# Kernel tuning notes

Hardware: AMD Instinct MI355X
Metric: run time of the kernel (lower is better)

## Reference

```python
import math
import jax, jax.numpy as jnp
import numpy as np
from jax import lax

CELL_SIZE = 8
N_BINS = 9
SIGNED = False


def _conv3x3(x, k):
    # x: [N,1,H,W], k: [1,1,3,3]; padding=1 (SAME), stride 1
    return lax.conv_general_dilated(
        x, k, window_strides=(1, 1), padding=[(1, 1), (1, 1)],
        dimension_numbers=("NCHW", "OIHW", "NCHW"))


def setup_inputs() -> dict:
    key = jax.random.key(0)
    x = jax.random.uniform(key, (64, 1, 512, 512), dtype=jnp.float32)
    sobel_x = jnp.array([[-1., 0., 1.], [-2., 0., 2.], [-1., 0., 1.]],
                        dtype=jnp.float32).reshape(1, 1, 3, 3)
    sobel_y = jnp.array([[-1., -2., -1.], [0., 0., 0.], [1., 2., 1.]],
                        dtype=jnp.float32).reshape(1, 1, 3, 3)
    return {"x": x, "sobel_x": sobel_x, "sobel_y": sobel_y}


def reference(x, sobel_x, sobel_y):
    n, _, H, W = x.shape
    angle_range = 2 * math.pi if SIGNED else math.pi

    gx = _conv3x3(x, sobel_x)  # [N,1,H,W]
    gy = _conv3x3(x, sobel_y)
    mag = jnp.sqrt(gx * gx + gy * gy)          # [N,1,H,W]
    ang = jnp.arctan2(gx, gy)                  # note: atan2(gx, gy) as in source
    ang = ang + math.pi if SIGNED else jnp.abs(ang)
    bins = jnp.floor(ang / angle_range * (N_BINS - 1)).astype(jnp.int32)  # [N,1,H,W]

    # scatter_(dim=1): one-hot write of magnitudes into bin channel
    onehot = jax.nn.one_hot(bins[:, 0], N_BINS, axis=1, dtype=mag.dtype)  # [N,nb,H,W]
    out = onehot * mag                                                     # [N,nb,H,W]

    # AvgPool2d(cell,stride=cell) * cell**2 == sum over each cell
    cs = CELL_SIZE
    hog = out.reshape(n, N_BINS, H // cs, cs, W // cs, cs).sum(axis=(3, 5))
    return hog.reshape(-1)
```

## Files before the change

### kernel.cpp

```cpp
#include <hip/hip_runtime.h>
#include <math.h>

#define IMG_H 512
#define IMG_W 512
#define NB 9

__global__ __launch_bounds__(256, 4) void hog_kernel(const float* __restrict__ x,
                                                     float* __restrict__ out) {
#pragma clang fp contract(off)
    const int tid  = threadIdx.x;
    const int w    = tid >> 6;
    const int lane = tid & 63;
    const int cl   = lane & 15;
    const int qid  = lane >> 4;
    const int sr   = qid >> 1;
    const int sc   = qid & 1;

    const int cx = (w << 4) | cl;
    const int cy = blockIdx.x;
    const int n  = blockIdx.y;

    const float* img = x + (size_t)n * (IMG_H * IMG_W);
    const int x0 = (cx << 3) + (sc << 2);
    const int y0 = (cy << 3) + (sr << 2);

    float r[6][6];
#pragma unroll
    for (int i = 0; i < 6; ++i) {
        const int y = y0 - 1 + i;
        if (y < 0 || y >= IMG_H) {
#pragma unroll
            for (int j = 0; j < 6; ++j) r[i][j] = 0.0f;
        } else {
            const float* row = img + (size_t)y * IMG_W;
            const float4 p = *(const float4*)(row + x0);
            r[i][1] = p.x; r[i][2] = p.y; r[i][3] = p.z; r[i][4] = p.w;
            r[i][0] = (x0 == 0)           ? 0.0f : row[x0 - 1];
            r[i][5] = (x0 + 4 >= IMG_W)   ? 0.0f : row[x0 + 4];
        }
    }

    float accA[4], accB[4], acc8;
#pragma unroll
    for (int k = 0; k < 4; ++k) { accA[k] = 0.0f; accB[k] = 0.0f; }
    acc8 = 0.0f;

    const float PI_F = 3.14159274101257324f;
    const float T1F  = 0.41421356237309503f;
    const float T3F  = 2.41421356237309503f;
    const float KPI  = 2.54647909f;
    const float EPS  = 5e-5f;

#pragma unroll
    for (int ry = 0; ry < 4; ++ry) {
#pragma unroll
        for (int j = 0; j < 4; ++j) {
            const float A0 = r[ry][j],     A1 = r[ry][j + 1], A2 = r[ry][j + 2];
            const float B0 = r[ry + 1][j],                    B2 = r[ry + 1][j + 2];
            const float C0 = r[ry + 2][j], C1 = r[ry + 2][j + 1], C2 = r[ry + 2][j + 2];

            const float gx = ((-A0 + (A2 - 2.0f * B0)) + (2.0f * B2 - C0)) + C2;
            const float gy = (((-A0 - 2.0f * A1) + (-A2)) + (C0 + 2.0f * C1)) + C2;

            const float u = fabsf(gx);
            const float W = fabsf(gy);
            const float q = u * u + W * W;
            const float mag = __builtin_amdgcn_sqrtf(q);

            const float b1 = W * T1F;
            const float b3 = W * T3F;
            const bool c1 = u > b1;
            const bool c2 = u > W;
            const bool c3 = u > b3;
            const bool s  = gy > 0.0f;

            const float KW = KPI * W;
            const float E  = EPS * q;
            const float md = fminf(fminf(fabsf(u - b1), fabsf(u - b3)),
                                   fminf(fabsf(u - W), u));
            const bool flag = md * KW < E;

            const float w0 = flag ? 0.0f : mag;
            const float wP = s ? w0 : 0.0f;
            const float wN = w0 - wP;
            const float p1 = c1 ? wP : 0.0f;
            const float p2 = c2 ? wP : 0.0f;
            const float p3 = c3 ? wP : 0.0f;
            const float n1 = c1 ? wN : 0.0f;
            const float n2 = c2 ? wN : 0.0f;
            const float n3 = c3 ? wN : 0.0f;
            accA[0] += wP - p1; accA[1] += p1 - p2;
            accA[2] += p2 - p3; accA[3] += p3;
            accB[0] += wN - n1; accB[1] += n1 - n2;
            accB[2] += n2 - n3; accB[3] += n3;

            if (flag) {
                const float angf = (float)atan2((double)u, (double)gy);
                const float tc = (float)((double)angf / (double)PI_F) * 8.0f;
                int bc = (int)tc;
                int bin = bc > 8 ? 8 : bc;
                float wA = mag;
                const float tn = roundf(tc);
                const int B = (int)tn;
                if (B >= 1 && B <= 8 && fabsf(tc - tn) < 4e-6f &&
                    mag <= 1.05f) {
                    const float hw = 0.5f * mag;
                    accA[0] += (B == 0) ? hw : 0.0f;
                    accA[1] += (B == 1) ? hw : 0.0f;
                    accA[2] += (B == 2) ? hw : 0.0f;
                    accA[3] += (B == 3) ? hw : 0.0f;
                    accB[3] += (B == 4) ? hw : 0.0f;
                    accB[2] += (B == 5) ? hw : 0.0f;
                    accB[1] += (B == 6) ? hw : 0.0f;
                    accB[0] += (B == 7) ? hw : 0.0f;
                    acc8    += (B == 8) ? hw : 0.0f;
                    bin = B - 1; wA = hw;
                }
                accA[0] += (bin == 0) ? wA : 0.0f;
                accA[1] += (bin == 1) ? wA : 0.0f;
                accA[2] += (bin == 2) ? wA : 0.0f;
                accA[3] += (bin == 3) ? wA : 0.0f;
                accB[3] += (bin == 4) ? wA : 0.0f;
                accB[2] += (bin == 5) ? wA : 0.0f;
                accB[1] += (bin == 6) ? wA : 0.0f;
                accB[0] += (bin == 7) ? wA : 0.0f;
                acc8    += (bin == 8) ? wA : 0.0f;
            }
        }
    }

    const float vals[NB] = {accA[0], accA[1], accA[2], accA[3],
                            accB[3], accB[2], accB[1], accB[0], acc8};
    float red[NB];
#pragma unroll
    for (int k = 0; k < NB; ++k) {
        float v = vals[k];
        v += __int_as_float(
                 __builtin_amdgcn_ds_swizzle(__float_as_int(v), 0x401F));
        v += __shfl_xor(v, 32, 64);
        red[k] = v;
    }

    const float v0 = qid == 0 ? red[0] : qid == 1 ? red[1]
                   : qid == 2 ? red[2] : red[3];
    const float v1 = qid == 0 ? red[4] : qid == 1 ? red[5]
                   : qid == 2 ? red[6] : red[7];
    float* o = out + (size_t)n * (NB * 64 * 64) + (size_t)cy * 64 + cx;
    o[(size_t)qid * 4096] = v0;
    o[(size_t)(qid + 4) * 4096] = v1;
    if (qid == 0) o[(size_t)8 * 4096] = red[8];
}

extern "C" void kernel_launch(void* const* d_in, const int* in_sizes, int n_in,
                              void* d_out, int out_size, void* d_ws, size_t ws_size,
                              hipStream_t stream) {
    const float* x = (const float*)d_in[0];
    float* out = (float*)d_out;
    hog_kernel<<<dim3(64, 64, 1), dim3(256, 1, 1), 0, stream>>>(x, out);
}
```

Baseline: 115.3 us.

## Use cumulative bin accumulators and defer rare exact-angle fallback to a masked pass

```diff
diff --git a/kernel.cpp b/kernel.cpp
--- a/kernel.cpp
+++ b/kernel.cpp
@@ -40,9 +40,9 @@
         }
     }
 
-    float accA[4], accB[4], acc8;
+    float accP[4], accN[4], acc8;
 #pragma unroll
-    for (int k = 0; k < 4; ++k) { accA[k] = 0.0f; accB[k] = 0.0f; }
+    for (int k = 0; k < 4; ++k) { accP[k] = 0.0f; accN[k] = 0.0f; }
     acc8 = 0.0f;
 
     const float PI_F = 3.14159274101257324f;
@@ -50,6 +50,8 @@
     const float T3F  = 2.41421356237309503f;
     const float KPI  = 2.54647909f;
     const float EPS  = 5e-5f;
+
+    unsigned msk = 0u;
 
 #pragma unroll
     for (int ry = 0; ry < 4; ++ry) {
@@ -79,58 +81,72 @@
             const float md = fminf(fminf(fabsf(u - b1), fabsf(u - b3)),
                                    fminf(fabsf(u - W), u));
             const bool flag = md * KW < E;
+            msk |= flag ? (1u << (ry * 4 + j)) : 0u;
 
             const float w0 = flag ? 0.0f : mag;
             const float wP = s ? w0 : 0.0f;
             const float wN = w0 - wP;
-            const float p1 = c1 ? wP : 0.0f;
-            const float p2 = c2 ? wP : 0.0f;
-            const float p3 = c3 ? wP : 0.0f;
-            const float n1 = c1 ? wN : 0.0f;
-            const float n2 = c2 ? wN : 0.0f;
-            const float n3 = c3 ? wN : 0.0f;
-            accA[0] += wP - p1; accA[1] += p1 - p2;
-            accA[2] += p2 - p3; accA[3] += p3;
-            accB[0] += wN - n1; accB[1] += n1 - n2;
-            accB[2] += n2 - n3; accB[3] += n3;
+            accP[0] += wP;
+            accP[1] += c1 ? wP : 0.0f;
+            accP[2] += c2 ? wP : 0.0f;
+            accP[3] += c3 ? wP : 0.0f;
+            accN[0] += wN;
+            accN[1] += c1 ? wN : 0.0f;
+            accN[2] += c2 ? wN : 0.0f;
+            accN[3] += c3 ? wN : 0.0f;
+        }
+    }
 
-            if (flag) {
-                const float angf = (float)atan2((double)u, (double)gy);
-                const float tc = (float)((double)angf / (double)PI_F) * 8.0f;
-                int bc = (int)tc;
-                int bin = bc > 8 ? 8 : bc;
-                float wA = mag;
-                const float tn = roundf(tc);
-                const int B = (int)tn;
-                if (B >= 1 && B <= 8 && fabsf(tc - tn) < 4e-6f &&
-                    mag <= 1.05f) {
-                    const float hw = 0.5f * mag;
-                    accA[0] += (B == 0) ? hw : 0.0f;
-                    accA[1] += (B == 1) ? hw : 0.0f;
-                    accA[2] += (B == 2) ? hw : 0.0f;
-                    accA[3] += (B == 3) ? hw : 0.0f;
-                    accB[3] += (B == 4) ? hw : 0.0f;
-                    accB[2] += (B == 5) ? hw : 0.0f;
-                    accB[1] += (B == 6) ? hw : 0.0f;
-                    accB[0] += (B == 7) ? hw : 0.0f;
-                    acc8    += (B == 8) ? hw : 0.0f;
-                    bin = B - 1; wA = hw;
+    if (msk) {
+        auto add_bin = [&](int b, float v) {
+            accP[0] += (b <= 3)           ? v : 0.0f;
+            accP[1] += (b >= 1 && b <= 3) ? v : 0.0f;
+            accP[2] += (b >= 2 && b <= 3) ? v : 0.0f;
+            accP[3] += (b == 3)           ? v : 0.0f;
+            accN[0] += (b >= 4 && b <= 7) ? v : 0.0f;
+            accN[1] += (b >= 4 && b <= 6) ? v : 0.0f;
+            accN[2] += (b >= 4 && b <= 5) ? v : 0.0f;
+            accN[3] += (b == 4)           ? v : 0.0f;
+            acc8    += (b == 8)           ? v : 0.0f;
+        };
+#pragma unroll
+        for (int ry = 0; ry < 4; ++ry) {
+#pragma unroll
+            for (int j = 0; j < 4; ++j) {
+                if (msk & (1u << (ry * 4 + j))) {
+                    const float A0 = r[ry][j],     A1 = r[ry][j + 1], A2 = r[ry][j + 2];
+                    const float B0 = r[ry + 1][j],                    B2 = r[ry + 1][j + 2];
+                    const float C0 = r[ry + 2][j], C1 = r[ry + 2][j + 1], C2 = r[ry + 2][j + 2];
+                    const float gx = ((-A0 + (A2 - 2.0f * B0)) + (2.0f * B2 - C0)) + C2;
+                    const float gy = (((-A0 - 2.0f * A1) + (-A2)) + (C0 + 2.0f * C1)) + C2;
+                    const float u = fabsf(gx);
+                    const float W = fabsf(gy);
+                    const float q = u * u + W * W;
+                    const float mag = __builtin_amdgcn_sqrtf(q);
+
+                    const float angf = (float)atan2((double)u, (double)gy);
+                    const float tc = (float)((double)angf / (double)PI_F) * 8.0f;
+                    int bc = (int)tc;
+                    int bin = bc > 8 ? 8 : bc;
+                    float wA = mag;
+                    const float tn = roundf(tc);
+                    const int B = (int)tn;
+                    if (B >= 1 && B <= 8 && fabsf(tc - tn) < 4e-6f &&
+                        mag <= 1.05f) {
+                        const float hw = 0.5f * mag;
+                        add_bin(B, hw);
+                        bin = B - 1; wA = hw;
+                    }
+                    add_bin(bin, wA);
                 }
-                accA[0] += (bin == 0) ? wA : 0.0f;
-                accA[1] += (bin == 1) ? wA : 0.0f;
-                accA[2] += (bin == 2) ? wA : 0.0f;
-                accA[3] += (bin == 3) ? wA : 0.0f;
-                accB[3] += (bin == 4) ? wA : 0.0f;
-                accB[2] += (bin == 5) ? wA : 0.0f;
-                accB[1] += (bin == 6) ? wA : 0.0f;
-                accB[0] += (bin == 7) ? wA : 0.0f;
-                acc8    += (bin == 8) ? wA : 0.0f;
             }
         }
     }
 
-    const float vals[NB] = {accA[0], accA[1], accA[2], accA[3],
-                            accB[3], accB[2], accB[1], accB[0], acc8};
+    const float vals[NB] = {accP[0] - accP[1], accP[1] - accP[2],
+                            accP[2] - accP[3], accP[3],
+                            accN[3],           accN[2] - accN[3],
+                            accN[1] - accN[2], accN[0] - accN[1], acc8};
     float red[NB];
 #pragma unroll
     for (int k = 0; k < NB; ++k) {
```

Result: no change. 113.1 us, median of 2 (-1.9%).
